# Performance work log

Hardware: AMD Instinct MI355X
Metric: run time of the kernel (lower is better)

Reference implementation:

```python
import jax, jax.numpy as jnp
import numpy as np

L, B, T, D, F = 2, 128, 512, 64, 512  # num_layers, batch, seq_len, input_dim, n_features


def setup_inputs() -> dict:
    key = jax.random.key(0)
    ks = jax.random.split(key, 16)
    s = 1.0 / np.sqrt(F)
    u = lambda k, shape: jax.random.uniform(k, shape, jnp.float32, -s, s)
    return {
        "x": jax.random.normal(ks[0], (L, B, D), jnp.float32),
        "last_feat": jax.random.normal(ks[1], (B, F), jnp.float32),
        "W_init": u(ks[2], (F, D)), "b_init": u(ks[3], (F,)),
        "W_ih0": u(ks[4], (4 * F, F)), "W_hh0": u(ks[5], (4 * F, F)),
        "b_ih0": u(ks[6], (4 * F,)), "b_hh0": u(ks[7], (4 * F,)),
        "W_ih1": u(ks[8], (4 * F, F)), "W_hh1": u(ks[9], (4 * F, F)),
        "b_ih1": u(ks[10], (4 * F,)), "b_hh1": u(ks[11], (4 * F,)),
        "W_out": u(ks[12], (F, F)), "b_out": u(ks[13], (F,)),
    }


def _lstm_cell(inp, h, c, W_ih, W_hh, b_ih, b_hh):
    # torch gate order: i, f, g, o
    gates = inp @ W_ih.T + b_ih + h @ W_hh.T + b_hh
    i, f, g, o = jnp.split(gates, 4, axis=-1)
    c_new = jax.nn.sigmoid(f) * c + jax.nn.sigmoid(i) * jnp.tanh(g)
    h_new = jax.nn.sigmoid(o) * jnp.tanh(c_new)
    return h_new, c_new


def reference(x, last_feat, W_init, b_init, W_ih0, W_hh0, b_ih0, b_hh0,
              W_ih1, W_hh1, b_ih1, b_hh1, W_out, b_out):
    # hidden and cell are BOTH initial_layer(x) -> identical initial states (L, B, F)
    h0 = x @ W_init.T + b_init
    c0 = h0

    def step(carry, _):
        out, h, c = carry  # out: (B,F); h,c: (L,B,F)
        h0n, c0n = _lstm_cell(out, h[0], c[0], W_ih0, W_hh0, b_ih0, b_hh0)
        h1n, c1n = _lstm_cell(h0n, h[1], c[1], W_ih1, W_hh1, b_ih1, b_hh1)
        # output_layer(out) in the original is computed but discarded (dead code)
        new_carry = (h1n, jnp.stack([h0n, h1n]), jnp.stack([c0n, c1n]))
        return new_carry, h1n

    _, outs = jax.lax.scan(step, (last_feat, h0, c0), None, length=T)  # (T, B, F)
    # faithful to torch: outputs.reshape((batch, seq_len, n_features)) — a raw reshape
    return outs.reshape(B, T, F)
```

## Files before the change

### kernel.cpp

```cpp
#include <hip/hip_runtime.h>
#include <hip/hip_bf16.h>

#define FDIM   512
#define BATCH  128
#define TSTEPS 512
#define GDIM   2048
#define NPH    (2*TSTEPS)

typedef __attribute__((ext_vector_type(8))) short bf16x8;
typedef __attribute__((ext_vector_type(4))) float f32x4;

union AfU { bf16x8 v; unsigned long long q[2]; };

__device__ __forceinline__ ushort f32_to_bf16(float v) {
    union { float f; unsigned u; } c; c.f = v;
    unsigned b = c.u;
    return (ushort)((b + 0x7FFFu + ((b >> 16) & 1u)) >> 16);
}
__device__ __forceinline__ float sigmoidf_(float x) { return 1.0f / (1.0f + expf(-x)); }

__device__ __forceinline__ unsigned long long aload64(const unsigned long long* p) {
    return __hip_atomic_load(p, __ATOMIC_RELAXED, __HIP_MEMORY_SCOPE_AGENT);
}
__device__ __forceinline__ unsigned aload32(const unsigned* p) {
    return __hip_atomic_load(p, __ATOMIC_RELAXED, __HIP_MEMORY_SCOPE_AGENT);
}
__device__ __forceinline__ void astore32(unsigned* p, unsigned v) {
    __hip_atomic_store(p, v, __ATOMIC_RELAXED, __HIP_MEMORY_SCOPE_AGENT);
}

__global__ __launch_bounds__(256) void convert_weights(
    const float* __restrict__ Wih0, const float* __restrict__ Whh0,
    const float* __restrict__ Wih1, const float* __restrict__ Whh1,
    const float* __restrict__ bih0, const float* __restrict__ bhh0,
    const float* __restrict__ bih1, const float* __restrict__ bhh1,
    ushort* __restrict__ wcat, float* __restrict__ bc)
{
    int idx = blockIdx.x * 256 + threadIdx.x;
    if (idx < 2 * GDIM * 1024) {
        int kk = idx & 1023;
        int r  = (idx >> 10) & 2047;
        int L  = idx >> 21;
        const float* Wih = L ? Wih1 : Wih0;
        const float* Whh = L ? Whh1 : Whh0;
        float v = (kk < 512) ? Wih[(size_t)r * 512 + kk] : Whh[(size_t)r * 512 + (kk - 512)];
        wcat[idx] = f32_to_bf16(v);
    }
    if (idx < 2 * GDIM) {
        int L = idx >> 11, r = idx & 2047;
        bc[idx] = L ? (bih1[r] + bhh1[r]) : (bih0[r] + bhh0[r]);
    }
}

__global__ __launch_bounds__(512, 2) void lstm_persistent(
    const float* __restrict__ x,
    const float* __restrict__ Winit,
    const float* __restrict__ binit,
    const float* __restrict__ lastf,
    const ushort* __restrict__ wcat,
    const float* __restrict__ bc,
    ushort* __restrict__ hst,
    ushort* __restrict__ lfbuf,
    unsigned* __restrict__ flags,
    float* __restrict__ out)
{
    const int tid  = threadIdx.x;
    const int lane = tid & 63;
    const int wave = tid >> 6;
    const int myL  = wave >> 2;
    const int kq   = wave & 3;
    const int g    = blockIdx.x & 7;
    const int ft   = blockIdx.x >> 3;
    const int wgid = g * 32 + ft;

    const int r16 = (tid >> 4) & 15;
    const int cc  = tid & 15;
    const int myB = g * 16 + r16;
    const int myF = ft * 16 + cc;

    __shared__ float part[4][4][16][16];

    float c_reg;
    {
        const float* xr = x + ((size_t)myL * BATCH + myB) * 64;
        const float* wr = Winit + (size_t)myF * 64;
        float s = binit[myF];
        #pragma unroll
        for (int k = 0; k < 64; ++k) s += xr[k] * wr[k];
        c_reg = s;
        unsigned hv = f32_to_bf16(s);
        unsigned up = (unsigned)__shfl_xor((int)hv, 1);
        if (!(cc & 1))
            astore32((unsigned*)(hst + (((size_t)myL * 2 + 1) * BATCH + myB) * FDIM + myF),
                     hv | (up << 16));
    }
    if (myL == 0) {
        float v = lastf[(size_t)myB * FDIM + myF];
        unsigned hv = f32_to_bf16(v);
        unsigned up = (unsigned)__shfl_xor((int)hv, 1);
        if (!(cc & 1))
            astore32((unsigned*)(lfbuf + (size_t)myB * FDIM + myF), hv | (up << 16));
    }
    float bias[4];
    #pragma unroll
    for (int ct = 0; ct < 4; ++ct) bias[ct] = bc[myL * GDIM + ct * FDIM + myF];

    bf16x8 bw[4][8];
    {
        const int wl = lane & 15, kg0 = lane >> 4;
        #pragma unroll
        for (int ct = 0; ct < 4; ++ct) {
            const ushort* base = wcat + ((size_t)myL * GDIM + ct * FDIM + ft * 16 + wl) * 1024
                               + kq * 256 + kg0 * 8;
            #pragma unroll
            for (int ks = 0; ks < 8; ++ks)
                bw[ct][ks] = *reinterpret_cast<const bf16x8*>(base + ks * 32);
        }
    }
    #pragma unroll
    for (int ct = 0; ct < 4; ++ct)
        #pragma unroll
        for (int ks = 0; ks < 8; ++ks)
            asm volatile("" : "+v"(bw[ct][ks]));

    __syncthreads();
    if (tid == 0) astore32(&flags[wgid], 1u);

    const int rA = lane & 15, kg = lane >> 4;

    for (int ph = 0; ph < NPH; ++ph) {
        const int L = ph & 1;
        const int t = ph >> 1;
        const bool active = (myL == L);

        const ushort* srcInp = (L == 0)
            ? (t == 0 ? lfbuf : hst + (size_t)(2 + ((t - 1) & 1)) * BATCH * FDIM)
            : (hst + (size_t)(t & 1) * BATCH * FDIM);
        const ushort* srcOwn = hst + (size_t)(L * 2 + ((t - 1) & 1)) * BATCH * FDIM;
        const ushort* arow = ((kq < 2) ? srcInp : srcOwn)
                           + (size_t)(g * 16 + rA) * FDIM + (kq & 1) * 256 + kg * 8;

        if (active) {
            if (kq < 2 || ph == 0) {
                const unsigned tgt = (unsigned)(ph + 1);
                const unsigned* fb = &flags[g * 32 + (kq & 1) * 16];
                for (;;) {
                    unsigned v = (lane < 16) ? aload32(&fb[lane]) : tgt;
                    if (__all((int)(v >= tgt))) break;
                }
            }
            bf16x8 af[8];
            #pragma unroll
            for (int ks = 0; ks < 8; ++ks) {
                AfU u;
                u.q[0] = aload64((const unsigned long long*)(arow + ks * 32));
                u.q[1] = aload64((const unsigned long long*)(arow + ks * 32) + 1);
                af[ks] = u.v;
            }
            f32x4 acc[4] = {{0,0,0,0},{0,0,0,0},{0,0,0,0},{0,0,0,0}};
            #pragma unroll
            for (int ks = 0; ks < 8; ++ks) {
                #pragma unroll
                for (int ct = 0; ct < 4; ++ct)
                    acc[ct] = __builtin_amdgcn_mfma_f32_16x16x32_bf16(af[ks], bw[ct][ks], acc[ct], 0, 0, 0);
            }
            const int n = lane & 15, q = lane >> 4;
            #pragma unroll
            for (int ct = 0; ct < 4; ++ct)
                #pragma unroll
                for (int j = 0; j < 4; ++j)
                    part[kq][ct][q * 4 + j][n] = acc[ct][j];
        }
        __syncthreads();

        if (active) {
            float gate[4];
            #pragma unroll
            for (int ct = 0; ct < 4; ++ct)
                gate[ct] = bias[ct] + part[0][ct][r16][cc] + part[1][ct][r16][cc]
                         + part[2][ct][r16][cc] + part[3][ct][r16][cc];
            float ig = sigmoidf_(gate[0]);
            float fg = sigmoidf_(gate[1]);
            float gg = tanhf(gate[2]);
            float og = sigmoidf_(gate[3]);
            float cn = fg * c_reg + ig * gg;
            float hn = og * tanhf(cn);
            c_reg = cn;
            unsigned hv = f32_to_bf16(hn);
            unsigned up = (unsigned)__shfl_xor((int)hv, 1);
            if (!(cc & 1))
                astore32((unsigned*)(hst + ((size_t)(L * 2 + (t & 1)) * BATCH + myB) * FDIM + myF),
                         hv | (up << 16));
            if (L == 1) out[((size_t)t * BATCH + myB) * FDIM + myF] = hn;
        }
        __syncthreads();
        if (tid == 0) astore32(&flags[wgid], (unsigned)(ph + 2));
    }
}

extern "C" void kernel_launch(void* const* d_in, const int* in_sizes, int n_in,
                              void* d_out, int out_size, void* d_ws, size_t ws_size,
                              hipStream_t stream)
{
    const float* x      = (const float*)d_in[0];
    const float* lastf  = (const float*)d_in[1];
    const float* W_init = (const float*)d_in[2];
    const float* b_init = (const float*)d_in[3];
    const float* W_ih0  = (const float*)d_in[4];
    const float* W_hh0  = (const float*)d_in[5];
    const float* b_ih0  = (const float*)d_in[6];
    const float* b_hh0  = (const float*)d_in[7];
    const float* W_ih1  = (const float*)d_in[8];
    const float* W_hh1  = (const float*)d_in[9];
    const float* b_ih1  = (const float*)d_in[10];
    const float* b_hh1  = (const float*)d_in[11];
    float* out = (float*)d_out;

    char* ws = (char*)d_ws;
    size_t off = 0;
    ushort*   wcat  = (ushort*)(ws + off);   off += (size_t)2 * GDIM * 1024 * 2;
    float*    bcb   = (float*)(ws + off);    off += (size_t)2 * GDIM * 4;
    ushort*   hstb  = (ushort*)(ws + off);   off += (size_t)2 * 2 * BATCH * FDIM * 2;
    ushort*   lfb   = (ushort*)(ws + off);   off += (size_t)BATCH * FDIM * 2;
    unsigned* flags = (unsigned*)(ws + off); off += 256 * 4;

    hipMemsetAsync(flags, 0, 256 * 4, stream);

    convert_weights<<<(2 * GDIM * 1024 + 255) / 256, 256, 0, stream>>>(
        W_ih0, W_hh0, W_ih1, W_hh1, b_ih0, b_hh0, b_ih1, b_hh1, wcat, bcb);

    lstm_persistent<<<256, 512, 0, stream>>>(
        x, W_init, b_init, lastf, wcat, bcb, hstb, lfb, flags, out);
}
```

Baseline: 3.551 ms.

## Replace flag-based inter-block barrier with poison-value data readiness polling

```diff
diff --git a/kernel.cpp b/kernel.cpp
--- a/kernel.cpp
+++ b/kernel.cpp
@@ -6,6 +6,8 @@
 #define TSTEPS 512
 #define GDIM   2048
 #define NPH    (2*TSTEPS)
+#define SLOT   (BATCH*FDIM)
+#define POISON 0xFFFFFFFFu
 
 typedef __attribute__((ext_vector_type(8))) short bf16x8;
 typedef __attribute__((ext_vector_type(4))) float f32x4;
@@ -22,10 +24,10 @@
 __device__ __forceinline__ unsigned long long aload64(const unsigned long long* p) {
     return __hip_atomic_load(p, __ATOMIC_RELAXED, __HIP_MEMORY_SCOPE_AGENT);
 }
-__device__ __forceinline__ unsigned aload32(const unsigned* p) {
-    return __hip_atomic_load(p, __ATOMIC_RELAXED, __HIP_MEMORY_SCOPE_AGENT);
-}
 __device__ __forceinline__ void astore32(unsigned* p, unsigned v) {
+    __hip_atomic_store(p, v, __ATOMIC_RELAXED, __HIP_MEMORY_SCOPE_AGENT);
+}
+__device__ __forceinline__ void astore64(unsigned long long* p, unsigned long long v) {
     __hip_atomic_store(p, v, __ATOMIC_RELAXED, __HIP_MEMORY_SCOPE_AGENT);
 }
 
@@ -59,9 +61,8 @@
     const float* __restrict__ lastf,
     const ushort* __restrict__ wcat,
     const float* __restrict__ bc,
-    ushort* __restrict__ hst,
+    ushort* __restrict__ hbuf,
     ushort* __restrict__ lfbuf,
-    unsigned* __restrict__ flags,
     float* __restrict__ out)
 {
     const int tid  = threadIdx.x;
@@ -71,14 +72,13 @@
     const int kq   = wave & 3;
     const int g    = blockIdx.x & 7;
     const int ft   = blockIdx.x >> 3;
-    const int wgid = g * 32 + ft;
 
     const int r16 = (tid >> 4) & 15;
     const int cc  = tid & 15;
     const int myB = g * 16 + r16;
     const int myF = ft * 16 + cc;
 
-    __shared__ float part[4][4][16][16];
+    __shared__ float part[2][4][4][16][16];
 
     float c_reg;
     {
@@ -91,7 +91,7 @@
         unsigned hv = f32_to_bf16(s);
         unsigned up = (unsigned)__shfl_xor((int)hv, 1);
         if (!(cc & 1))
-            astore32((unsigned*)(hst + (((size_t)myL * 2 + 1) * BATCH + myB) * FDIM + myF),
+            astore32((unsigned*)(hbuf + (size_t)(2 + myL) * SLOT + myB * FDIM + myF),
                      hv | (up << 16));
     }
     if (myL == 0) {
@@ -123,9 +123,6 @@
         for (int ks = 0; ks < 8; ++ks)
             asm volatile("" : "+v"(bw[ct][ks]));
 
-    __syncthreads();
-    if (tid == 0) astore32(&flags[wgid], 1u);
-
     const int rA = lane & 15, kg = lane >> 4;
 
     for (int ph = 0; ph < NPH; ++ph) {
@@ -133,30 +130,27 @@
         const int t = ph >> 1;
         const bool active = (myL == L);
 
-        const ushort* srcInp = (L == 0)
-            ? (t == 0 ? lfbuf : hst + (size_t)(2 + ((t - 1) & 1)) * BATCH * FDIM)
-            : (hst + (size_t)(t & 1) * BATCH * FDIM);
-        const ushort* srcOwn = hst + (size_t)(L * 2 + ((t - 1) & 1)) * BATCH * FDIM;
-        const ushort* arow = ((kq < 2) ? srcInp : srcOwn)
-                           + (size_t)(g * 16 + rA) * FDIM + (kq & 1) * 256 + kg * 8;
-
         if (active) {
-            if (kq < 2 || ph == 0) {
-                const unsigned tgt = (unsigned)(ph + 1);
-                const unsigned* fb = &flags[g * 32 + (kq & 1) * 16];
-                for (;;) {
-                    unsigned v = (lane < 16) ? aload32(&fb[lane]) : tgt;
-                    if (__all((int)(v >= tgt))) break;
+            const ushort* srcBase = (kq < 2)
+                ? ((ph == 0) ? lfbuf : hbuf + (size_t)((ph + 3) & 3) * SLOT)
+                : (hbuf + (size_t)((ph + 2) & 3) * SLOT);
+            const ushort* arow = srcBase + (size_t)(g * 16 + rA) * FDIM + (kq & 1) * 256 + kg * 8;
+
+            bf16x8 af[8];
+            for (;;) {
+                bool ok = true;
+                #pragma unroll
+                for (int ks = 0; ks < 8; ++ks) {
+                    AfU u;
+                    u.q[0] = aload64((const unsigned long long*)(arow + ks * 32));
+                    u.q[1] = aload64((const unsigned long long*)(arow + ks * 32) + 1);
+                    af[ks] = u.v;
+                    ok = ok && ((unsigned)u.q[0] != POISON) && ((unsigned)(u.q[0] >> 32) != POISON)
+                            && ((unsigned)u.q[1] != POISON) && ((unsigned)(u.q[1] >> 32) != POISON);
                 }
+                if (__all((int)ok)) break;
             }
-            bf16x8 af[8];
-            #pragma unroll
-            for (int ks = 0; ks < 8; ++ks) {
-                AfU u;
-                u.q[0] = aload64((const unsigned long long*)(arow + ks * 32));
-                u.q[1] = aload64((const unsigned long long*)(arow + ks * 32) + 1);
-                af[ks] = u.v;
-            }
+
             f32x4 acc[4] = {{0,0,0,0},{0,0,0,0},{0,0,0,0},{0,0,0,0}};
             #pragma unroll
             for (int ks = 0; ks < 8; ++ks) {
@@ -169,7 +163,7 @@
             for (int ct = 0; ct < 4; ++ct)
                 #pragma unroll
                 for (int j = 0; j < 4; ++j)
-                    part[kq][ct][q * 4 + j][n] = acc[ct][j];
+                    part[ph & 1][kq][ct][q * 4 + j][n] = acc[ct][j];
         }
         __syncthreads();
 
@@ -177,8 +171,9 @@
             float gate[4];
             #pragma unroll
             for (int ct = 0; ct < 4; ++ct)
-                gate[ct] = bias[ct] + part[0][ct][r16][cc] + part[1][ct][r16][cc]
-                         + part[2][ct][r16][cc] + part[3][ct][r16][cc];
+                gate[ct] = bias[ct]
+                         + part[ph & 1][0][ct][r16][cc] + part[ph & 1][1][ct][r16][cc]
+                         + part[ph & 1][2][ct][r16][cc] + part[ph & 1][3][ct][r16][cc];
             float ig = sigmoidf_(gate[0]);
             float fg = sigmoidf_(gate[1]);
             float gg = tanhf(gate[2]);
@@ -189,12 +184,19 @@
             unsigned hv = f32_to_bf16(hn);
             unsigned up = (unsigned)__shfl_xor((int)hv, 1);
             if (!(cc & 1))
-                astore32((unsigned*)(hst + ((size_t)(L * 2 + (t & 1)) * BATCH + myB) * FDIM + myF),
+                astore32((unsigned*)(hbuf + (size_t)(ph & 3) * SLOT + myB * FDIM + myF),
                          hv | (up << 16));
             if (L == 1) out[((size_t)t * BATCH + myB) * FDIM + myF] = hn;
+
+            if (kq == 0) {
+                unsigned* ptile = (unsigned*)(hbuf + (size_t)((ph + 1) & 3) * SLOT);
+                int idx = lane * 2;
+                int row = idx >> 3;
+                int dc  = idx & 7;
+                astore64((unsigned long long*)(ptile + (size_t)(g * 16 + row) * 256 + ft * 8 + dc),
+                         0xFFFFFFFFFFFFFFFFull);
+            }
         }
-        __syncthreads();
-        if (tid == 0) astore32(&flags[wgid], (unsigned)(ph + 2));
     }
 }
 
@@ -218,17 +220,16 @@
 
     char* ws = (char*)d_ws;
     size_t off = 0;
-    ushort*   wcat  = (ushort*)(ws + off);   off += (size_t)2 * GDIM * 1024 * 2;
-    float*    bcb   = (float*)(ws + off);    off += (size_t)2 * GDIM * 4;
-    ushort*   hstb  = (ushort*)(ws + off);   off += (size_t)2 * 2 * BATCH * FDIM * 2;
-    ushort*   lfb   = (ushort*)(ws + off);   off += (size_t)BATCH * FDIM * 2;
-    unsigned* flags = (unsigned*)(ws + off); off += 256 * 4;
-
-    hipMemsetAsync(flags, 0, 256 * 4, stream);
+    ushort* wcat = (ushort*)(ws + off); off += (size_t)2 * GDIM * 1024 * 2;
+    float*  bcb  = (float*)(ws + off);  off += (size_t)2 * GDIM * 4;
+    ushort* hbuf = (ushort*)(ws + off); off += (size_t)4 * SLOT * 2;
+    ushort* lfb  = (ushort*)(ws + off); off += (size_t)SLOT * 2;
+
+    hipMemsetAsync(hbuf, 0xFF, (size_t)5 * SLOT * 2, stream);
 
     convert_weights<<<(2 * GDIM * 1024 + 255) / 256, 256, 0, stream>>>(
         W_ih0, W_hh0, W_ih1, W_hh1, b_ih0, b_hh0, b_ih1, b_hh1, wcat, bcb);
 
     lstm_persistent<<<256, 512, 0, stream>>>(
-        x, W_init, b_init, lastf, wcat, bcb, hstb, lfb, flags, out);
-}
+        x, W_init, b_init, lastf, wcat, bcb, hbuf, lfb, out);
+}
```

Result: slower. 6.571 ms (+85.1%).

## Replace per-workgroup flags with per-group atomic counters and drop trailing barrier

Applied to the files above, without the earlier changes.

```diff
diff --git a/kernel.cpp b/kernel.cpp
--- a/kernel.cpp
+++ b/kernel.cpp
@@ -6,6 +6,7 @@
 #define TSTEPS 512
 #define GDIM   2048
 #define NPH    (2*TSTEPS)
+#define SLOT   (BATCH*FDIM)
 
 typedef __attribute__((ext_vector_type(8))) short bf16x8;
 typedef __attribute__((ext_vector_type(4))) float f32x4;
@@ -17,7 +18,12 @@
     unsigned b = c.u;
     return (ushort)((b + 0x7FFFu + ((b >> 16) & 1u)) >> 16);
 }
-__device__ __forceinline__ float sigmoidf_(float x) { return 1.0f / (1.0f + expf(-x)); }
+__device__ __forceinline__ float fsigmoid(float x) {
+    return __fdividef(1.0f, 1.0f + __expf(-x));
+}
+__device__ __forceinline__ float ftanh(float x) {
+    return 1.0f - __fdividef(2.0f, __expf(2.0f * x) + 1.0f);
+}
 
 __device__ __forceinline__ unsigned long long aload64(const unsigned long long* p) {
     return __hip_atomic_load(p, __ATOMIC_RELAXED, __HIP_MEMORY_SCOPE_AGENT);
@@ -61,7 +67,7 @@
     const float* __restrict__ bc,
     ushort* __restrict__ hst,
     ushort* __restrict__ lfbuf,
-    unsigned* __restrict__ flags,
+    unsigned* __restrict__ gcnt,
     float* __restrict__ out)
 {
     const int tid  = threadIdx.x;
@@ -71,14 +77,15 @@
     const int kq   = wave & 3;
     const int g    = blockIdx.x & 7;
     const int ft   = blockIdx.x >> 3;
-    const int wgid = g * 32 + ft;
 
     const int r16 = (tid >> 4) & 15;
     const int cc  = tid & 15;
     const int myB = g * 16 + r16;
     const int myF = ft * 16 + cc;
 
-    __shared__ float part[4][4][16][16];
+    unsigned* gc = gcnt + g * 32;
+
+    __shared__ float part[2][4][4][16][16];
 
     float c_reg;
     {
@@ -124,7 +131,8 @@
             asm volatile("" : "+v"(bw[ct][ks]));
 
     __syncthreads();
-    if (tid == 0) astore32(&flags[wgid], 1u);
+    if (tid == 0)
+        __hip_atomic_fetch_add(gc, 4u, __ATOMIC_RELAXED, __HIP_MEMORY_SCOPE_AGENT);
 
     const int rA = lane & 15, kg = lane >> 4;
 
@@ -132,23 +140,21 @@
         const int L = ph & 1;
         const int t = ph >> 1;
         const bool active = (myL == L);
-
-        const ushort* srcInp = (L == 0)
-            ? (t == 0 ? lfbuf : hst + (size_t)(2 + ((t - 1) & 1)) * BATCH * FDIM)
-            : (hst + (size_t)(t & 1) * BATCH * FDIM);
-        const ushort* srcOwn = hst + (size_t)(L * 2 + ((t - 1) & 1)) * BATCH * FDIM;
-        const ushort* arow = ((kq < 2) ? srcInp : srcOwn)
-                           + (size_t)(g * 16 + rA) * FDIM + (kq & 1) * 256 + kg * 8;
+        const int pb = ph & 1;
 
         if (active) {
+            const ushort* srcBase = (kq < 2)
+                ? ((ph == 0) ? lfbuf
+                   : (L == 0 ? hst + (size_t)(2 + ((t - 1) & 1)) * SLOT
+                             : hst + (size_t)(t & 1) * SLOT))
+                : (hst + (size_t)(L * 2 + ((t - 1) & 1)) * SLOT);
+            const ushort* arow = srcBase + (size_t)(g * 16 + rA) * FDIM + (kq & 1) * 256 + kg * 8;
+
             if (kq < 2 || ph == 0) {
-                const unsigned tgt = (unsigned)(ph + 1);
-                const unsigned* fb = &flags[g * 32 + (kq & 1) * 16];
-                for (;;) {
-                    unsigned v = (lane < 16) ? aload32(&fb[lane]) : tgt;
-                    if (__all((int)(v >= tgt))) break;
-                }
+                const unsigned tgt = 128u * (unsigned)(ph + 1);
+                while (aload32(gc) < tgt) {}
             }
+
             bf16x8 af[8];
             #pragma unroll
             for (int ks = 0; ks < 8; ++ks) {
@@ -169,7 +175,7 @@
             for (int ct = 0; ct < 4; ++ct)
                 #pragma unroll
                 for (int j = 0; j < 4; ++j)
-                    part[kq][ct][q * 4 + j][n] = acc[ct][j];
+                    part[pb][kq][ct][q * 4 + j][n] = acc[ct][j];
         }
         __syncthreads();
 
@@ -177,24 +183,25 @@
             float gate[4];
             #pragma unroll
             for (int ct = 0; ct < 4; ++ct)
-                gate[ct] = bias[ct] + part[0][ct][r16][cc] + part[1][ct][r16][cc]
-                         + part[2][ct][r16][cc] + part[3][ct][r16][cc];
-            float ig = sigmoidf_(gate[0]);
-            float fg = sigmoidf_(gate[1]);
-            float gg = tanhf(gate[2]);
-            float og = sigmoidf_(gate[3]);
+                gate[ct] = bias[ct] + part[pb][0][ct][r16][cc] + part[pb][1][ct][r16][cc]
+                         + part[pb][2][ct][r16][cc] + part[pb][3][ct][r16][cc];
+            float ig = fsigmoid(gate[0]);
+            float fg = fsigmoid(gate[1]);
+            float gg = ftanh(gate[2]);
+            float og = fsigmoid(gate[3]);
             float cn = fg * c_reg + ig * gg;
-            float hn = og * tanhf(cn);
+            float hn = og * ftanh(cn);
             c_reg = cn;
             unsigned hv = f32_to_bf16(hn);
             unsigned up = (unsigned)__shfl_xor((int)hv, 1);
             if (!(cc & 1))
                 astore32((unsigned*)(hst + ((size_t)(L * 2 + (t & 1)) * BATCH + myB) * FDIM + myF),
                          hv | (up << 16));
+            asm volatile("s_waitcnt vmcnt(0)" ::: "memory");
+            if (lane == 0)
+                __hip_atomic_fetch_add(gc, 1u, __ATOMIC_RELAXED, __HIP_MEMORY_SCOPE_AGENT);
             if (L == 1) out[((size_t)t * BATCH + myB) * FDIM + myF] = hn;
         }
-        __syncthreads();
-        if (tid == 0) astore32(&flags[wgid], (unsigned)(ph + 2));
     }
 }
 
@@ -218,17 +225,17 @@
 
     char* ws = (char*)d_ws;
     size_t off = 0;
-    ushort*   wcat  = (ushort*)(ws + off);   off += (size_t)2 * GDIM * 1024 * 2;
-    float*    bcb   = (float*)(ws + off);    off += (size_t)2 * GDIM * 4;
-    ushort*   hstb  = (ushort*)(ws + off);   off += (size_t)2 * 2 * BATCH * FDIM * 2;
-    ushort*   lfb   = (ushort*)(ws + off);   off += (size_t)BATCH * FDIM * 2;
-    unsigned* flags = (unsigned*)(ws + off); off += 256 * 4;
-
-    hipMemsetAsync(flags, 0, 256 * 4, stream);
+    ushort*   wcat = (ushort*)(ws + off);   off += (size_t)2 * GDIM * 1024 * 2;
+    float*    bcb  = (float*)(ws + off);    off += (size_t)2 * GDIM * 4;
+    ushort*   hstb = (ushort*)(ws + off);   off += (size_t)2 * 2 * BATCH * FDIM * 2;
+    ushort*   lfb  = (ushort*)(ws + off);   off += (size_t)BATCH * FDIM * 2;
+    unsigned* gcnt = (unsigned*)(ws + off); off += (size_t)8 * 32 * 4;
+
+    hipMemsetAsync(gcnt, 0, (size_t)8 * 32 * 4, stream);
 
     convert_weights<<<(2 * GDIM * 1024 + 255) / 256, 256, 0, stream>>>(
         W_ih0, W_hh0, W_ih1, W_hh1, b_ih0, b_hh0, b_ih1, b_hh1, wcat, bcb);
 
     lstm_persistent<<<256, 512, 0, stream>>>(
-        x, W_init, b_init, lastf, wcat, bcb, hstb, lfb, flags, out);
-}
+        x, W_init, b_init, lastf, wcat, bcb, hstb, lfb, gcnt, out);
+}
```

Result: slower. 6.540 ms (+84.2%).
